# Performance work log

Measured on AMD Instinct MI355X. Metric: run time of the kernel, lower is better.

Reference implementation:

```python
import jax, jax.numpy as jnp
import numpy as np

N, M, N0 = 100000, 12, 2500            # atoms, max neighbors, crystals
ORIG, C, NBR, H, NCONV = 92, 64, 41, 128, 3
EPS = 1e-5                              # torch BatchNorm1d default eps


def setup_inputs() -> dict:
    key = jax.random.key(0)
    ks = jax.random.split(key, 10)
    return {
        "atom_fea": jax.random.normal(ks[0], (N, ORIG), jnp.float32),
        "nbr_fea": jax.random.normal(ks[1], (N, M, NBR), jnp.float32),
        "nbr_fea_idx": jax.random.randint(ks[2], (N, M), 0, N),
        "crystal_atom_idx": jnp.sort(jax.random.randint(ks[3], (N,), 0, N0)),
        # learned parameters (Linear weights stored as (in, out))
        "emb_W": jax.random.normal(ks[4], (ORIG, C), jnp.float32) * 0.05,
        "emb_b": jnp.zeros((C,), jnp.float32),
        "fc_W": jax.random.normal(ks[5], (NCONV, 2 * C + NBR, 2 * C), jnp.float32) * 0.05,
        "fc_b": jnp.zeros((NCONV, 2 * C), jnp.float32),
        "bn1_g": jnp.ones((NCONV, 2 * C), jnp.float32),
        "bn1_b": jnp.zeros((NCONV, 2 * C), jnp.float32),
        "bn2_g": jnp.ones((NCONV, C), jnp.float32),
        "bn2_b": jnp.zeros((NCONV, C), jnp.float32),
        "head_W": jax.random.normal(ks[6], (C, H), jnp.float32) * 0.05,
        "head_b": jnp.zeros((H,), jnp.float32),
        "out_W": jax.random.normal(ks[7], (H, 1), jnp.float32) * 0.05,
        "out_b": jnp.zeros((1,), jnp.float32),
    }


def _bn(x, g, b):
    # training-mode BatchNorm1d: per-feature batch mean/var (biased)
    mu = jnp.mean(x, axis=0)
    var = jnp.var(x, axis=0)
    return (x - mu) * jax.lax.rsqrt(var + EPS) * g + b


def reference(atom_fea, nbr_fea, nbr_fea_idx, crystal_atom_idx,
              emb_W, emb_b, fc_W, fc_b, bn1_g, bn1_b, bn2_g, bn2_b,
              head_W, head_b, out_W, out_b):
    h = atom_fea @ emb_W + emb_b                       # (N, C)
    for l in range(NCONV):
        nbr_h = h[nbr_fea_idx]                         # gather (N, M, C)
        self_h = jnp.broadcast_to(h[:, None, :], (N, M, C))
        tot = jnp.concatenate([self_h, nbr_h, nbr_fea], axis=2)  # (N, M, 2C+NBR)
        g = tot @ fc_W[l] + fc_b[l]                    # (N, M, 2C)
        g = _bn(g.reshape(-1, 2 * C), bn1_g[l], bn1_b[l]).reshape(N, M, 2 * C)
        filt = jax.nn.sigmoid(g[..., :C])
        core = jax.nn.softplus(g[..., C:])
        summed = jnp.sum(filt * core, axis=1)          # (N, C)
        summed = _bn(summed, bn2_g[l], bn2_b[l])
        h = jax.nn.softplus(h + summed)                # residual
    # per-crystal mean pooling via segment sum
    counts = jax.ops.segment_sum(jnp.ones((N,), h.dtype), crystal_atom_idx, num_segments=N0)
    crys = jax.ops.segment_sum(h, crystal_atom_idx, num_segments=N0) / jnp.maximum(counts, 1.0)[:, None]
    z = jax.nn.softplus(jax.nn.softplus(crys) @ head_W + head_b)  # (N0, H)
    return z @ out_W + out_b                            # (N0, 1)
```

## Files before the change

### kernel.cpp

```cpp
#include <hip/hip_runtime.h>

#define NA 100000
#define MN 12
#define KE 41
#define N0C 2500
#define EPSBN 1e-5f
#define ROWDW 24
#define CONV_BLOCKS 1024
#define CONV_WAVES (CONV_BLOCKS * 4)

typedef _Float16 h2v __attribute__((ext_vector_type(2)));
typedef _Float16 h8v __attribute__((ext_vector_type(8)));
typedef float f4v __attribute__((ext_vector_type(4)));
typedef unsigned int uint;
union H2U { uint u; h2v h; };

__device__ __forceinline__ float softplusf(float x){
  float e = __expf(-fabsf(x));
  return fmaxf(x, 0.f) + __logf(1.f + e);
}
__device__ __forceinline__ float sigmoidf(float x){
  return __fdividef(1.f, 1.f + __expf(-x));
}
__device__ __forceinline__ int waveid(){
  return __builtin_amdgcn_readfirstlane((int)((blockIdx.x * blockDim.x + threadIdx.x) >> 6));
}

__global__ __launch_bounds__(256) void k_cast_e(const float* __restrict__ e,
                                                uint* __restrict__ EF)
{
  const int TOT = NA * MN * ROWDW;
  for (int i = blockIdx.x * 256 + threadIdx.x; i < TOT; i += gridDim.x * 256) {
    int r = i / ROWDW, k2 = i - r * ROWDW;
    const float* row = e + (size_t)r * KE;
    float a = 0.f, b = 0.f;
    if (k2 < 20) { a = row[2 * k2]; b = row[2 * k2 + 1]; }
    else if (k2 == 20) { a = row[40]; }
    H2U cv; cv.h = h2v{(_Float16)a, (_Float16)b};
    EF[i] = cv.u;
  }
}

__global__ __launch_bounds__(256) void k_embed(const float* __restrict__ af,
                                               const float* __restrict__ W,
                                               const float* __restrict__ b,
                                               float* __restrict__ h, int nw)
{
  int t = threadIdx.x & 63;
  int wid = waveid();
  float bias = b[t];
  for (int n0 = wid * 2; n0 < NA; n0 += nw * 2) {
    int n1 = n0 + 1;
    bool has1 = (n1 < NA);
    const float* a0 = af + (size_t)n0 * 92;
    const float* a1 = af + (size_t)(has1 ? n1 : n0) * 92;
    float acc0 = bias, acc1 = bias;
#pragma unroll 4
    for (int k = 0; k < 92; ++k) {
      float w = W[k * 64 + t];
      acc0 += a0[k] * w;
      acc1 += a1[k] * w;
    }
    h[(size_t)n0 * 64 + t] = acc0;
    if (has1) h[(size_t)n1 * 64 + t] = acc1;
  }
}

__global__ __launch_bounds__(256) void k_hw(const float* __restrict__ h,
                                            const float* __restrict__ fcW,
                                            uint* __restrict__ hWs,
                                            uint* __restrict__ hWn, int nw)
{
  __shared__ float Wl[64 * 256];
  for (int i = threadIdx.x; i < 64 * 256; i += 256) {
    int c = i >> 8, q = i & 255;
    int j = q & 63, part = q >> 6;
    Wl[(c * 64 + j) * 4 + part] = fcW[(c + ((part >> 1) << 6)) * 128 + ((part & 1) << 6) + j];
  }
  __syncthreads();
  int t = threadIdx.x & 63;
  int wid = waveid();
  const float4* W4 = (const float4*)Wl;
  for (int n0 = wid * 2; n0 < NA; n0 += nw * 2) {
    int n1 = n0 + 1;
    bool has1 = (n1 < NA);
    const float* ha = h + (size_t)n0 * 64;
    const float* hb = h + (size_t)(has1 ? n1 : n0) * 64;
    float4 A = {0,0,0,0}, B = {0,0,0,0};
#pragma unroll 4
    for (int c = 0; c < 64; ++c) {
      float4 w = W4[c * 64 + t];
      float x0 = ha[c], x1 = hb[c];
      A.x += x0 * w.x; A.y += x0 * w.y; A.z += x0 * w.z; A.w += x0 * w.w;
      B.x += x1 * w.x; B.y += x1 * w.y; B.z += x1 * w.z; B.w += x1 * w.w;
    }
    H2U p0, p1;
    p0.h = h2v{(_Float16)A.x, (_Float16)A.y};
    p1.h = h2v{(_Float16)A.z, (_Float16)A.w};
    hWs[(size_t)n0 * 64 + t] = p0.u;
    hWn[(size_t)n0 * 64 + t] = p1.u;
    if (has1) {
      p0.h = h2v{(_Float16)B.x, (_Float16)B.y};
      p1.h = h2v{(_Float16)B.z, (_Float16)B.w};
      hWs[(size_t)n1 * 64 + t] = p0.u;
      hWn[(size_t)n1 * 64 + t] = p1.u;
    }
  }
}

template<int APPLY>
__global__ __launch_bounds__(256) void k_conv(const uint* __restrict__ EF,
                                              const uint* __restrict__ hWs,
                                              const uint* __restrict__ hWn,
                                              const int*  __restrict__ idx,
                                              const float* __restrict__ We,
                                              const float* __restrict__ scsh,
                                              float* __restrict__ summed,
                                              float* __restrict__ stats)
{
  __shared__ float gt_all[4][16 * 132];
  int l = threadIdx.x & 63;
  int w = threadIdx.x >> 6;
  float* gt = gt_all[w];
  int wid = __builtin_amdgcn_readfirstlane(blockIdx.x * 4 + w);
  int c16 = l & 15, kg = l >> 4;

  h8v b1[8], b2[8];
#pragma unroll
  for (int T = 0; T < 8; ++T) {
    h8v v1 = {0,0,0,0,0,0,0,0}, v2 = {0,0,0,0,0,0,0,0};
#pragma unroll
    for (int j = 0; j < 8; ++j)
      v1[j] = (_Float16)We[(kg * 8 + j) * 128 + T * 16 + c16];
    if (kg < 2) {
#pragma unroll
      for (int j = 0; j < 8; ++j) {
        int k = 32 + kg * 8 + j;
        v2[j] = (k < KE) ? (_Float16)We[k * 128 + T * 16 + c16] : (_Float16)0.f;
      }
    }
    b1[T] = v1; b2[T] = v2;
  }

  float sc0 = 0, sh0 = 0, sc1 = 0, sh1 = 0;
  if (APPLY) { sc0 = scsh[l]; sc1 = scsh[l + 64]; sh0 = scsh[128 + l]; sh1 = scsh[192 + l]; }
  float s0 = 0, q0 = 0, s1 = 0, q1 = 0;

  for (int n = wid; n < NA; n += CONV_WAVES) {
    const uint* ep = EF + (size_t)n * (MN * ROWDW);
    h8v a1 = {0,0,0,0,0,0,0,0}, a2 = {0,0,0,0,0,0,0,0};
    if (c16 < MN) {
      a1 = *(const h8v*)(ep + c16 * ROWDW + kg * 4);
      if (kg < 2) a2 = *(const h8v*)(ep + c16 * ROWDW + 16 + kg * 4);
    }
    f4v acc[8];
#pragma unroll
    for (int T = 0; T < 8; ++T) acc[T] = f4v{0.f, 0.f, 0.f, 0.f};
#pragma unroll
    for (int T = 0; T < 8; ++T)
      acc[T] = __builtin_amdgcn_mfma_f32_16x16x32_f16(a1, b1[T], acc[T], 0, 0, 0);
#pragma unroll
    for (int T = 0; T < 8; ++T)
      acc[T] = __builtin_amdgcn_mfma_f32_16x16x32_f16(a2, b2[T], acc[T], 0, 0, 0);

#pragma unroll
    for (int T = 0; T < 8; ++T)
#pragma unroll
      for (int r = 0; r < 4; ++r)
        gt[(kg * 4 + r) * 132 + T * 16 + c16] = acc[T][r];

    const int* ip = idx + n * MN;
    H2U sp; sp.u = hWs[(size_t)n * 64 + l];
    float self0 = (float)sp.h[0], self1 = (float)sp.h[1];
    uint nbp[MN];
#pragma unroll
    for (int m = 0; m < MN; ++m) nbp[m] = hWn[(size_t)ip[m] * 64 + l];
    float accsum = 0.f;
#pragma unroll
    for (int m = 0; m < MN; ++m) {
      H2U nv; nv.u = nbp[m];
      float g0 = gt[m * 132 + l]      + self0 + (float)nv.h[0];
      float g1 = gt[m * 132 + 64 + l] + self1 + (float)nv.h[1];
      if (APPLY) {
        float f  = sigmoidf(g0 * sc0 + sh0);
        float cr = softplusf(g1 * sc1 + sh1);
        accsum += f * cr;
      } else {
        s0 += g0; q0 += g0 * g0;
        s1 += g1; q1 += g1 * g1;
      }
    }
    if (APPLY) {
      summed[(size_t)n * 64 + l] = accsum;
      s0 += accsum; q0 += accsum * accsum;
    }
  }
  if (APPLY) {
    atomicAdd(&stats[l], s0);
    atomicAdd(&stats[64 + l], q0);
  } else {
    atomicAdd(&stats[l], s0);
    atomicAdd(&stats[64 + l], s1);
    atomicAdd(&stats[128 + l], q0);
    atomicAdd(&stats[192 + l], q1);
  }
}

__global__ void k_fin1(const float* __restrict__ st, const float* __restrict__ g,
                       const float* __restrict__ b, float* __restrict__ scsh)
{
  int j = threadIdx.x;
  float inv = 1.f / (float)(NA * MN);
  float mean = st[j] * inv;
  float var  = st[128 + j] * inv - mean * mean;
  float rstd = rsqrtf(var + EPSBN);
  float sc = g[j] * rstd;
  scsh[j] = sc;
  scsh[128 + j] = b[j] - mean * sc;
}
__global__ void k_fin2(const float* __restrict__ st, const float* __restrict__ g,
                       const float* __restrict__ b, float* __restrict__ scsh)
{
  int j = threadIdx.x;
  float inv = 1.f / (float)NA;
  float mean = st[j] * inv;
  float var  = st[64 + j] * inv - mean * mean;
  float rstd = rsqrtf(var + EPSBN);
  float sc = g[j] * rstd;
  scsh[j] = sc;
  scsh[64 + j] = b[j] - mean * sc;
}

__global__ __launch_bounds__(256) void k_bn2res(float* __restrict__ h,
                                                const float* __restrict__ summed,
                                                const float* __restrict__ scsh)
{
  int tot = NA * 64 / 4;
  const float4* s4 = (const float4*)summed;
  float4* h4 = (float4*)h;
  for (int i = blockIdx.x * blockDim.x + threadIdx.x; i < tot; i += gridDim.x * blockDim.x) {
    int c4 = i & 15;
    float4 sc = ((const float4*)scsh)[c4];
    float4 sh = ((const float4*)(scsh + 64))[c4];
    float4 hv = h4[i], sv = s4[i];
    hv.x = softplusf(hv.x + sv.x * sc.x + sh.x);
    hv.y = softplusf(hv.y + sv.y * sc.y + sh.y);
    hv.z = softplusf(hv.z + sv.z * sc.z + sh.z);
    hv.w = softplusf(hv.w + sv.w * sc.w + sh.w);
    h4[i] = hv;
  }
}

__global__ __launch_bounds__(256) void k_pool(const float* __restrict__ h,
                                              const int* __restrict__ cidx,
                                              float* __restrict__ csum,
                                              float* __restrict__ ccnt, int nw)
{
  int t = threadIdx.x & 63;
  int wid = waveid();
  int chunk = (NA + nw - 1) / nw;
  int n0 = wid * chunk;
  int n1 = min(n0 + chunk, NA);
  if (n0 >= NA) return;
  float acc = 0.f, cacc = 0.f;
  int cur = -1;
  for (int n = n0; n < n1; ++n) {
    int ci = cidx[n];
    if (ci != cur) {
      if (cur >= 0) {
        atomicAdd(&csum[(size_t)cur * 64 + t], acc);
        if (t == 0) atomicAdd(&ccnt[cur], cacc);
      }
      cur = ci; acc = 0.f; cacc = 0.f;
    }
    acc += h[(size_t)n * 64 + t];
    cacc += 1.f;
  }
  if (cur >= 0) {
    atomicAdd(&csum[(size_t)cur * 64 + t], acc);
    if (t == 0) atomicAdd(&ccnt[cur], cacc);
  }
}

__global__ __launch_bounds__(256) void k_head(const float* __restrict__ csum,
                                              const float* __restrict__ ccnt,
                                              const float* __restrict__ Wh,
                                              const float* __restrict__ bh,
                                              const float* __restrict__ Wo,
                                              const float* __restrict__ bo,
                                              float* __restrict__ out)
{
  __shared__ float Wl[64 * 128];
  for (int i = threadIdx.x; i < 64 * 128; i += 256) Wl[i] = Wh[i];
  __syncthreads();
  int t = threadIdx.x & 63;
  int ci = blockIdx.x * 4 + (threadIdx.x >> 6);
  if (ci >= N0C) return;
  float cnt = fmaxf(ccnt[ci], 1.f);
  float x = softplusf(csum[(size_t)ci * 64 + t] / cnt);
  float acc0 = 0.f, acc1 = 0.f;
#pragma unroll 4
  for (int c = 0; c < 64; ++c) {
    float xc = __shfl(x, c, 64);
    acc0 += xc * Wl[c * 128 + t];
    acc1 += xc * Wl[c * 128 + 64 + t];
  }
  float z0 = softplusf(acc0 + bh[t]);
  float z1 = softplusf(acc1 + bh[64 + t]);
  float part = z0 * Wo[t] + z1 * Wo[64 + t];
#pragma unroll
  for (int s = 32; s >= 1; s >>= 1) part += __shfl_xor(part, s, 64);
  if (t == 0) out[ci] = part + bo[0];
}

extern "C" void kernel_launch(void* const* d_in, const int* in_sizes, int n_in,
                              void* d_out, int out_size, void* d_ws, size_t ws_size,
                              hipStream_t stream)
{
  const float* af    = (const float*)d_in[0];
  const float* nbr   = (const float*)d_in[1];
  const int*   nidx  = (const int*)d_in[2];
  const int*   cidx  = (const int*)d_in[3];
  const float* embW  = (const float*)d_in[4];
  const float* embB  = (const float*)d_in[5];
  const float* fcW   = (const float*)d_in[6];
  const float* bn1g  = (const float*)d_in[8];
  const float* bn1b  = (const float*)d_in[9];
  const float* bn2g  = (const float*)d_in[10];
  const float* bn2b  = (const float*)d_in[11];
  const float* headW = (const float*)d_in[12];
  const float* headB = (const float*)d_in[13];
  const float* outW  = (const float*)d_in[14];
  const float* outB  = (const float*)d_in[15];
  float* out = (float*)d_out;

  float* ws = (float*)d_ws;
  size_t off = 0;
  float* h      = ws + off; off += (size_t)NA * 64;
  uint*  hWs    = (uint*)(ws + off); off += (size_t)NA * 64;
  uint*  hWn    = (uint*)(ws + off); off += (size_t)NA * 64;
  uint*  EF     = (uint*)(ws + off); off += (size_t)NA * MN * ROWDW;
  float* summed = ws + off; off += (size_t)NA * 64;
  float* zr     = ws + off;
  float* stats1 = zr;
  float* stats2 = stats1 + 3 * 256;
  float* csum   = stats2 + 3 * 128;
  float* ccnt   = csum + (size_t)N0C * 64;
  size_t zcount = 3 * 256 + 3 * 128 + (size_t)N0C * 64 + N0C;
  float* scsh1  = ccnt + N0C;
  float* scsh2  = scsh1 + 3 * 256;

  hipMemsetAsync(zr, 0, zcount * sizeof(float), stream);

  k_cast_e<<<4096, 256, 0, stream>>>(nbr, EF);
  k_embed<<<512, 256, 0, stream>>>(af, embW, embB, h, 2048);

  for (int l = 0; l < 3; ++l) {
    const float* Wl = fcW + (size_t)l * 169 * 128;
    const float* We = Wl + 128 * 128;
    k_hw<<<512, 256, 0, stream>>>(h, Wl, hWs, hWn, 2048);
    k_conv<0><<<CONV_BLOCKS, 256, 0, stream>>>(EF, hWs, hWn, nidx, We, nullptr, nullptr,
                                               stats1 + l * 256);
    k_fin1<<<1, 128, 0, stream>>>(stats1 + l * 256, bn1g + l * 128, bn1b + l * 128,
                                  scsh1 + l * 256);
    k_conv<1><<<CONV_BLOCKS, 256, 0, stream>>>(EF, hWs, hWn, nidx, We, scsh1 + l * 256,
                                               summed, stats2 + l * 128);
    k_fin2<<<1, 64, 0, stream>>>(stats2 + l * 128, bn2g + l * 64, bn2b + l * 64,
                                 scsh2 + l * 128);
    k_bn2res<<<2048, 256, 0, stream>>>(h, summed, scsh2 + l * 128);
  }

  k_pool<<<512, 256, 0, stream>>>(h, cidx, csum, ccnt, 2048);
  k_head<<<625, 256, 0, stream>>>(csum, ccnt, headW, headB, outW, outB, out);
}
```

Baseline: 1.624 ms.

## Fuse BN2 residual into next layer's hW kernel, prefetch gathers, trim LDS

For layers after the first, the BN2+residual+softplus update is folded into the k_hw kernel, which now computes the new h in registers, writes it back, and broadcasts it with wave shuffles instead of rereading rows from memory. Only the final layer keeps a separate k_bn2res launch. The conv kernel now issues its neighbor gathers before the MFMAs so their latency can overlap with compute, and it stores only the 12 used rows to a smaller LDS tile. The conv grid size is also raised. Together these aim to cut kernel launches, global traffic and LDS use, at the cost of more register pressure in k_conv.

```diff
diff --git a/kernel.cpp b/kernel.cpp
--- a/kernel.cpp
+++ b/kernel.cpp
@@ -6,7 +6,7 @@
 #define N0C 2500
 #define EPSBN 1e-5f
 #define ROWDW 24
-#define CONV_BLOCKS 1024
+#define CONV_BLOCKS 1536
 #define CONV_WAVES (CONV_BLOCKS * 4)
 
 typedef _Float16 h2v __attribute__((ext_vector_type(2)));
@@ -66,7 +66,10 @@
   }
 }
 
-__global__ __launch_bounds__(256) void k_hw(const float* __restrict__ h,
+template<int FUSE>
+__global__ __launch_bounds__(256) void k_hw(float* __restrict__ h,
+                                            const float* __restrict__ summed,
+                                            const float* __restrict__ scsh2,
                                             const float* __restrict__ fcW,
                                             uint* __restrict__ hWs,
                                             uint* __restrict__ hWn, int nw)
@@ -80,17 +83,26 @@
   __syncthreads();
   int t = threadIdx.x & 63;
   int wid = waveid();
+  float sc = 0.f, sh = 0.f;
+  if (FUSE) { sc = scsh2[t]; sh = scsh2[64 + t]; }
   const float4* W4 = (const float4*)Wl;
   for (int n0 = wid * 2; n0 < NA; n0 += nw * 2) {
     int n1 = n0 + 1;
     bool has1 = (n1 < NA);
-    const float* ha = h + (size_t)n0 * 64;
-    const float* hb = h + (size_t)(has1 ? n1 : n0) * 64;
+    float hf0 = h[(size_t)n0 * 64 + t];
+    float hf1 = h[(size_t)(has1 ? n1 : n0) * 64 + t];
+    if (FUSE) {
+      hf0 = softplusf(hf0 + summed[(size_t)n0 * 64 + t] * sc + sh);
+      hf1 = softplusf(hf1 + summed[(size_t)(has1 ? n1 : n0) * 64 + t] * sc + sh);
+      h[(size_t)n0 * 64 + t] = hf0;
+      if (has1) h[(size_t)n1 * 64 + t] = hf1;
+    }
     float4 A = {0,0,0,0}, B = {0,0,0,0};
 #pragma unroll 4
     for (int c = 0; c < 64; ++c) {
       float4 w = W4[c * 64 + t];
-      float x0 = ha[c], x1 = hb[c];
+      float x0 = __shfl(hf0, c, 64);
+      float x1 = __shfl(hf1, c, 64);
       A.x += x0 * w.x; A.y += x0 * w.y; A.z += x0 * w.z; A.w += x0 * w.w;
       B.x += x1 * w.x; B.y += x1 * w.y; B.z += x1 * w.z; B.w += x1 * w.w;
     }
@@ -118,7 +130,7 @@
                                               float* __restrict__ summed,
                                               float* __restrict__ stats)
 {
-  __shared__ float gt_all[4][16 * 132];
+  __shared__ float gt_all[4][12 * 132];
   int l = threadIdx.x & 63;
   int w = threadIdx.x >> 6;
   float* gt = gt_all[w];
@@ -153,6 +165,12 @@
       a1 = *(const h8v*)(ep + c16 * ROWDW + kg * 4);
       if (kg < 2) a2 = *(const h8v*)(ep + c16 * ROWDW + 16 + kg * 4);
     }
+    const int* ip = idx + n * MN;
+    H2U sp; sp.u = hWs[(size_t)n * 64 + l];
+    uint nbp[MN];
+#pragma unroll
+    for (int m = 0; m < MN; ++m) nbp[m] = hWn[(size_t)ip[m] * 64 + l];
+
     f4v acc[8];
 #pragma unroll
     for (int T = 0; T < 8; ++T) acc[T] = f4v{0.f, 0.f, 0.f, 0.f};
@@ -163,18 +181,15 @@
     for (int T = 0; T < 8; ++T)
       acc[T] = __builtin_amdgcn_mfma_f32_16x16x32_f16(a2, b2[T], acc[T], 0, 0, 0);
 
-#pragma unroll
-    for (int T = 0; T < 8; ++T)
-#pragma unroll
-      for (int r = 0; r < 4; ++r)
-        gt[(kg * 4 + r) * 132 + T * 16 + c16] = acc[T][r];
-
-    const int* ip = idx + n * MN;
-    H2U sp; sp.u = hWs[(size_t)n * 64 + l];
+    if (kg < 3) {
+#pragma unroll
+      for (int T = 0; T < 8; ++T)
+#pragma unroll
+        for (int r = 0; r < 4; ++r)
+          gt[(kg * 4 + r) * 132 + T * 16 + c16] = acc[T][r];
+    }
+
     float self0 = (float)sp.h[0], self1 = (float)sp.h[1];
-    uint nbp[MN];
-#pragma unroll
-    for (int m = 0; m < MN; ++m) nbp[m] = hWn[(size_t)ip[m] * 64 + l];
     float accsum = 0.f;
 #pragma unroll
     for (int m = 0; m < MN; ++m) {
@@ -358,18 +373,21 @@
   for (int l = 0; l < 3; ++l) {
     const float* Wl = fcW + (size_t)l * 169 * 128;
     const float* We = Wl + 128 * 128;
-    k_hw<<<512, 256, 0, stream>>>(h, Wl, hWs, hWn, 2048);
-    k_conv<0><<<CONV_BLOCKS, 256, 0, stream>>>(EF, hWs, hWn, nidx, We, nullptr, nullptr,
-                                               stats1 + l * 256);
+    if (l == 0)
+      k_hw<0><<<512, 256, 0, stream>>>(h, nullptr, nullptr, Wl, hWs, hWn, 2048);
+    else
+      k_hw<1><<<512, 256, 0, stream>>>(h, summed, scsh2 + (l - 1) * 128, Wl, hWs, hWn, 2048);
+    k_conv<0><<<CONV_BLOCKS, 256, 0, stream>>>(EF, hWs, hWn, nidx, We, nullptr,
+                                               nullptr, stats1 + l * 256);
     k_fin1<<<1, 128, 0, stream>>>(stats1 + l * 256, bn1g + l * 128, bn1b + l * 128,
                                   scsh1 + l * 256);
     k_conv<1><<<CONV_BLOCKS, 256, 0, stream>>>(EF, hWs, hWn, nidx, We, scsh1 + l * 256,
                                                summed, stats2 + l * 128);
     k_fin2<<<1, 64, 0, stream>>>(stats2 + l * 128, bn2g + l * 64, bn2b + l * 64,
                                  scsh2 + l * 128);
-    k_bn2res<<<2048, 256, 0, stream>>>(h, summed, scsh2 + l * 128);
-  }
-
+  }
+
+  k_bn2res<<<2048, 256, 0, stream>>>(h, summed, scsh2 + 2 * 128);
   k_pool<<<512, 256, 0, stream>>>(h, cidx, csum, ccnt, 2048);
   k_head<<<625, 256, 0, stream>>>(csum, ccnt, headW, headB, outW, outB, out);
 }
```

After: 1.855 ms. +14.2%, slower.
